# Kernel tuning notes

Hardware: AMD Instinct MI355X
Metric: run time of the kernel (lower is better)

The kernel has to match this reference:

```python
import jax, jax.numpy as jnp
import numpy as np

B, L, R, F, E, H, A, V = 256, 24, 49, 2048, 256, 512, 512, 10000


def setup_inputs() -> dict:
    key = jax.random.key(0)
    ks = jax.random.split(key, 16)
    w = lambda k, shape: jax.random.normal(k, shape, jnp.float32) * 0.02
    feats = jax.random.normal(ks[0], (B, R, F), jnp.float32)
    captions_ids = jax.random.randint(ks[1], (B, L), 0, V).astype(jnp.int32)
    # descending-sorted lengths in [2, L], max forced to L (packed-batch convention)
    lengths = jnp.sort(jax.random.randint(ks[2], (B,), 2, L + 1))[::-1].astype(jnp.int32)
    lengths = lengths.at[0].set(L)
    return {
        "feats": feats,
        "captions_ids": captions_ids,
        "lengths": lengths,
        "embed_W": w(ks[3], (V, E)),
        "Wf": w(ks[4], (A, F)), "bf": jnp.zeros((A,), jnp.float32),
        "Wh": w(ks[5], (A, H)), "bh": jnp.zeros((A,), jnp.float32),
        "Ws": w(ks[6], (1, A)), "bs": jnp.zeros((1,), jnp.float32),
        "W_ih": w(ks[7], (4 * H, E + F)), "b_ih": jnp.zeros((4 * H,), jnp.float32),
        "W_hh": w(ks[8], (4 * H, H)), "b_hh": jnp.zeros((4 * H,), jnp.float32),
        "Wfc": w(ks[9], (V, H)), "bfc": jnp.zeros((V,), jnp.float32),
        "Wi_h": w(ks[10], (H, F)), "bi_h": jnp.zeros((H,), jnp.float32),
        "Wi_c": w(ks[11], (H, F)), "bi_c": jnp.zeros((H,), jnp.float32),
    }


def reference(feats, captions_ids, lengths, embed_W, Wf, bf, Wh, bh, Ws, bs,
              W_ih, b_ih, W_hh, b_hh, Wfc, bfc, Wi_h, bi_h, Wi_c, bi_c):
    # init state from mean-pooled features
    mean = feats.mean(axis=1)                       # (B, F)
    h0 = jnp.tanh(mean @ Wi_h.T + bi_h)             # (B, H)
    c0 = jnp.tanh(mean @ Wi_c.T + bi_c)
    emb = embed_W[captions_ids]                     # (B, L, E)
    f_proj = feats @ Wf.T + bf                      # (B, R, A) hoisted out of loop
    steps = captions_ids.shape[1] - 1

    def step(carry, xs):
        h, c = carry
        emb_t, t = xs                               # (B, E), scalar
        # soft attention
        hp = h @ Wh.T + bh                          # (B, A)
        e = jnp.tanh(f_proj + hp[:, None, :])       # (B, R, A)
        scores = e @ Ws[0] + bs[0]                  # (B, R)
        alpha = jax.nn.softmax(scores, axis=1)
        ctx = jnp.einsum('br,brf->bf', alpha, feats)  # (B, F)
        # LSTMCell (torch gate order i,f,g,o); dropout is identity in eval
        x = jnp.concatenate([emb_t, ctx], axis=1)   # (B, E+F)
        gates = x @ W_ih.T + b_ih + h @ W_hh.T + b_hh
        i, f, g, o = jnp.split(gates, 4, axis=1)
        i, f, o = jax.nn.sigmoid(i), jax.nn.sigmoid(f), jax.nn.sigmoid(o)
        g = jnp.tanh(g)
        c_t = f * c + i * g
        h_t = o * jnp.tanh(c_t)
        # ragged masking: only rows with lengths > t are active this step
        mask = (lengths > t)[:, None]
        h = jnp.where(mask, h_t, h)
        c = jnp.where(mask, c_t, c)
        logit = jnp.where(mask, h_t @ Wfc.T + bfc, 0.0)  # (B, V); zeros for padded rows
        return (h, c), logit

    xs = (jnp.swapaxes(emb[:, :steps], 0, 1), jnp.arange(steps))
    _, logits = jax.lax.scan(step, (h0, c0), xs)    # (steps, B, V)
    return jnp.swapaxes(logits, 0, 1)               # (B, steps, V)
```

## Files before the change

kernel.cpp:

```cpp
#include <hip/hip_runtime.h>

constexpr int Bc = 256, Lc = 24, Rc = 49, Fc = 2048, Ec = 256, Hc = 512, Acn = 512, Vc = 10000;
constexpr int STEPS = Lc - 1;
constexpr int XE = Ec + Fc;
constexpr int NG = 2048 + Acn;
constexpr int VPAD = 10112;

using bf16x8  = __attribute__((ext_vector_type(8))) __bf16;
using floatx4 = __attribute__((ext_vector_type(4))) float;
using ushort8 = __attribute__((ext_vector_type(8))) unsigned short;
using ushort4v = __attribute__((ext_vector_type(4))) unsigned short;

__device__ inline float bf2f(unsigned short u) {
    unsigned int x = ((unsigned int)u) << 16;
    float f; __builtin_memcpy(&f, &x, sizeof(f)); return f;
}
__device__ inline unsigned short f2bf(float f) {
    unsigned int u; __builtin_memcpy(&u, &f, sizeof(u));
    u += 0x7fffu + ((u >> 16) & 1u);
    return (unsigned short)(u >> 16);
}

__device__ inline void gload_lds16(const void* g, void* l) {
    __builtin_amdgcn_global_load_lds(
        (const __attribute__((address_space(1))) unsigned int*)g,
        (__attribute__((address_space(3))) unsigned int*)l, 16, 0, 0);
}

struct CvtArgs {
    const float* src[9];
    unsigned short* dst[9];
};
constexpr int SEG_END[9] = {
    6422528,
    7062528,
    7324672,
    8604672,
    9784320,
    10046464,
    10112000,
    10374144,
    10636288
};
constexpr int CVT_BLOCKS = SEG_END[8] / 256;

__global__ __launch_bounds__(256) void convert_all(CvtArgs a)
{
    int g = blockIdx.x * 256 + threadIdx.x;
    int s = 0, base = 0;
    #pragma unroll
    for (int i = 0; i < 9; i++)
        if (g >= SEG_END[i]) { s = i + 1; }
    if (s >= 9) return;
    base = (s == 0) ? 0 : SEG_END[s - 1];
    const float* sp = a.src[s];
    unsigned short* dp = a.dst[s];
    int off = g - base;
    float4 v = reinterpret_cast<const float4*>(sp)[off];
    ushort4v o;
    o.x = f2bf(v.x); o.y = f2bf(v.y); o.z = f2bf(v.z); o.w = f2bf(v.w);
    reinterpret_cast<ushort4v*>(dp)[off] = o;
}

template <int BM, int BN, int BK, int EPI>
__global__ __launch_bounds__(256) void gemm_tn(
    const unsigned short* __restrict__ A, int lda,
    const unsigned short* __restrict__ Bm, int ldb,
    const unsigned short* __restrict__ Bm2,
    const float* __restrict__ bias,
    const float* __restrict__ bias2,
    float* __restrict__ outF,
    unsigned short* __restrict__ outU,
    float* __restrict__ outF2,
    int N, int K)
{
    static_assert(BK == 64, "row must be 128B for the swizzle");
    __shared__ __align__(16) unsigned short smem[(BM + BN) * BK];
    unsigned short* sA = smem;
    unsigned short* sB = smem + BM * BK;

    const int tid = threadIdx.x;
    const int wid = tid >> 6, lane = tid & 63;
    const int wm = wid >> 1, wn = wid & 1;
    const int m0 = blockIdx.x * BM, n0 = blockIdx.y * BN;
    constexpr int FM = BM / 32, FN = (BN + 31) / 32;
    constexpr int ACH = BM / 32;
    constexpr int BCH = BN / 32;

    floatx4 acc[FM][FN];
    #pragma unroll
    for (int i = 0; i < FM; i++)
        #pragma unroll
        for (int j = 0; j < FN; j++)
            #pragma unroll
            for (int r = 0; r < 4; r++) acc[i][j][r] = 0.f;

    const int lm = lane & 15, half = lane >> 4;
    const int lane16 = lane * 16;

    for (int k0 = 0; k0 < K; k0 += BK) {
        #pragma unroll
        for (int ii = 0; ii < ACH; ii++) {
            int ldso = (wid * ACH + ii) * 1024 + lane16;
            int row = ldso >> 7, colb = ldso & 127;
            int scolb = colb ^ ((row & 7) << 4);
            const char* src = (const char*)(A + (size_t)(m0 + row) * lda + k0) + scolb;
            gload_lds16(src, (char*)sA + ldso);
        }
        #pragma unroll
        for (int ii = 0; ii < BCH; ii++) {
            int ldso = (wid * BCH + ii) * 1024 + lane16;
            int row = ldso >> 7, colb = ldso & 127;
            int scolb = colb ^ ((row & 7) << 4);
            int gn = n0 + row;
            const unsigned short* bp;
            if constexpr (EPI == 2)
                bp = (gn < Hc) ? (Bm + (size_t)gn * ldb) : (Bm2 + (size_t)(gn - Hc) * ldb);
            else
                bp = Bm + (size_t)gn * ldb;
            gload_lds16((const char*)(bp + k0) + scolb, (char*)sB + ldso);
        }
        __syncthreads();

        #pragma unroll
        for (int kk = 0; kk < BK; kk += 32) {
            bf16x8 af[FM], bfb[FN];
            #pragma unroll
            for (int fm = 0; fm < FM; fm++) {
                int ar = wm * (BM / 2) + fm * 16 + lm;
                int ab = ar * 128 + ((kk * 2 + half * 16) ^ ((ar & 7) << 4));
                af[fm] = *reinterpret_cast<const bf16x8*>((const char*)sA + ab);
            }
            #pragma unroll
            for (int fn = 0; fn < FN; fn++) {
                int br = wn * (BN / 2) + fn * 16 + lm;
                int bb = br * 128 + ((kk * 2 + half * 16) ^ ((br & 7) << 4));
                bfb[fn] = *reinterpret_cast<const bf16x8*>((const char*)sB + bb);
            }
            #pragma unroll
            for (int fm = 0; fm < FM; fm++)
                #pragma unroll
                for (int fn = 0; fn < FN; fn++)
                    acc[fm][fn] = __builtin_amdgcn_mfma_f32_16x16x32_bf16(
                        af[fm], bfb[fn], acc[fm][fn], 0, 0, 0);
        }
        __syncthreads();
    }

    const int quad = lane >> 4;
    #pragma unroll
    for (int fm = 0; fm < FM; fm++) {
        #pragma unroll
        for (int fn = 0; fn < FN; fn++) {
            #pragma unroll
            for (int r = 0; r < 4; r++) {
                int rowG = m0 + wm * (BM / 2) + fm * 16 + quad * 4 + r;
                int colG = n0 + wn * (BN / 2) + fn * 16 + lm;
                float v = acc[fm][fn][r];
                if constexpr (EPI == 0) {
                    if (bias) v += bias[colG];
                    outF[(size_t)rowG * N + colG] = v;
                } else if constexpr (EPI == 1) {
                    if (bias) v += bias[colG];
                    outU[(size_t)rowG * N + colG] = f2bf(v);
                } else if constexpr (EPI == 2) {
                    float b = (colG < Hc) ? bias[colG] : bias2[colG - Hc];
                    v = tanhf(v + b);
                    if (colG < Hc) outU[(size_t)rowG * Hc + colG] = f2bf(v);
                    else           outF2[(size_t)rowG * Hc + (colG - Hc)] = v;
                }
            }
        }
    }
}

__global__ __launch_bounds__(256) void logits_gemm(
    const unsigned short* __restrict__ A,
    const unsigned short* __restrict__ Bm,
    const float* __restrict__ bias,
    float* __restrict__ out,
    const int* __restrict__ lengths)
{
    constexpr int BM = 128, BN = 64, BK = 64, K = Hc;
    constexpr int EP = 68;
    __shared__ __align__(16) unsigned char smraw[BM * EP * 4];
    unsigned short* sA = (unsigned short*)smraw;
    unsigned short* sB = sA + BM * BK;
    float* sE = (float*)smraw;

    const int tid = threadIdx.x;
    const int wid = tid >> 6, lane = tid & 63;
    const int wm = wid >> 1, wn = wid & 1;

    constexpr int NWG = 46 * 157, NX = 8;
    constexpr int qq = NWG / NX, rr = NWG % NX;
    int wg = blockIdx.x + blockIdx.y * 46;
    int xcd = wg % NX, i = wg / NX;
    int w = (xcd < rr ? xcd * (qq + 1) : rr * (qq + 1) + (xcd - rr) * qq) + i;
    const int m0 = (w % 46) * BM, n0 = (w / 46) * BN;
    constexpr int FM = 4, FN = 2;

    const int rl = lane >> 4, cl = lane & 15;
    const int colG = n0 + cl * 4;
    const bool colOK = colG < Vc;

    const int tt0 = m0 >> 8;
    if (lengths[m0 & 255] <= tt0) {
        if (colOK) {
            float4 z; z.x = 0.f; z.y = 0.f; z.z = 0.f; z.w = 0.f;
            #pragma unroll
            for (int it = 0; it < 8; it++) {
                int r = wid * 32 + it * 4 + rl;
                int bb = (m0 + r) & 255;
                *reinterpret_cast<float4*>(
                    out + ((size_t)bb * STEPS + tt0) * Vc + colG) = z;
            }
        }
        return;
    }

    floatx4 acc[FM][FN];
    #pragma unroll
    for (int i2 = 0; i2 < FM; i2++)
        #pragma unroll
        for (int j = 0; j < FN; j++)
            #pragma unroll
            for (int r = 0; r < 4; r++) acc[i2][j][r] = 0.f;

    const int lm = lane & 15, half = lane >> 4;
    const int lane16 = lane * 16;

    for (int k0 = 0; k0 < K; k0 += BK) {
        #pragma unroll
        for (int ii = 0; ii < 4; ii++) {
            int ldso = (wid * 4 + ii) * 1024 + lane16;
            int row = ldso >> 7, colb = ldso & 127;
            int scolb = colb ^ ((row & 7) << 4);
            const char* src = (const char*)(A + (size_t)(m0 + row) * K + k0) + scolb;
            gload_lds16(src, (char*)sA + ldso);
        }
        #pragma unroll
        for (int ii = 0; ii < 2; ii++) {
            int ldso = (wid * 2 + ii) * 1024 + lane16;
            int row = ldso >> 7, colb = ldso & 127;
            int scolb = colb ^ ((row & 7) << 4);
            const char* src = (const char*)(Bm + (size_t)(n0 + row) * K + k0) + scolb;
            gload_lds16(src, (char*)sB + ldso);
        }
        __syncthreads();

        #pragma unroll
        for (int kk = 0; kk < BK; kk += 32) {
            bf16x8 af[FM], bfb[FN];
            #pragma unroll
            for (int fm = 0; fm < FM; fm++) {
                int ar = wm * 64 + fm * 16 + lm;
                int ab = ar * 128 + ((kk * 2 + half * 16) ^ ((ar & 7) << 4));
                af[fm] = *reinterpret_cast<const bf16x8*>((const char*)sA + ab);
            }
            #pragma unroll
            for (int fn = 0; fn < FN; fn++) {
                int br = wn * 32 + fn * 16 + lm;
                int bb = br * 128 + ((kk * 2 + half * 16) ^ ((br & 7) << 4));
                bfb[fn] = *reinterpret_cast<const bf16x8*>((const char*)sB + bb);
            }
            #pragma unroll
            for (int fm = 0; fm < FM; fm++)
                #pragma unroll
                for (int fn = 0; fn < FN; fn++)
                    acc[fm][fn] = __builtin_amdgcn_mfma_f32_16x16x32_bf16(
                        af[fm], bfb[fn], acc[fm][fn], 0, 0, 0);
        }
        __syncthreads();
    }

    const int quad = lane >> 4;
    #pragma unroll
    for (int fm = 0; fm < FM; fm++)
        #pragma unroll
        for (int fn = 0; fn < FN; fn++)
            #pragma unroll
            for (int r = 0; r < 4; r++)
                sE[(wm * 64 + fm * 16 + quad * 4 + r) * EP + wn * 32 + fn * 16 + lm]
                    = acc[fm][fn][r];
    __syncthreads();

    if (colOK) {
        float4 bv = *reinterpret_cast<const float4*>(bias + colG);
        #pragma unroll
        for (int it = 0; it < 8; it++) {
            int r = wid * 32 + it * 4 + rl;
            int rowG = m0 + r;
            int tt = rowG >> 8, bb = rowG & 255;
            bool act = lengths[bb] > tt;
            float4 v = *reinterpret_cast<const float4*>(sE + r * EP + cl * 4);
            float4 o;
            o.x = act ? v.x + bv.x : 0.f;
            o.y = act ? v.y + bv.y : 0.f;
            o.z = act ? v.z + bv.z : 0.f;
            o.w = act ? v.w + bv.w : 0.f;
            *reinterpret_cast<float4*>(out + ((size_t)bb * STEPS + tt) * Vc + colG) = o;
        }
    }
}

__global__ __launch_bounds__(256) void attn_lstm_kernel(
    const unsigned short* __restrict__ fproj,
    const unsigned short* __restrict__ fprojG,
    const unsigned short* __restrict__ embProj,
    const float* __restrict__ hg,
    const float* __restrict__ bh,
    const float* __restrict__ Ws,
    const float* __restrict__ bs,
    const float* __restrict__ b_ih,
    const float* __restrict__ b_hh,
    float* __restrict__ c_state,
    unsigned short* __restrict__ h_buf,
    unsigned short* __restrict__ h_all,
    const int* __restrict__ lengths,
    const int* __restrict__ ids,
    int t)
{
    const int b = blockIdx.x, tid = threadIdx.x;
    const int wid = tid >> 6, lane = tid & 63;
    __shared__ float s_hp[Acn];
    __shared__ float s_sc[64];
    __shared__ float s_g[2048];

    #pragma unroll
    for (int i = tid; i < Acn; i += 256)
        s_hp[i] = hg[(size_t)b * NG + 2048 + i] + bh[i];
    __syncthreads();

    float ws8[8], hp8[8];
    {
        const float* wsb = Ws + lane * 8;
        #pragma unroll
        for (int j = 0; j < 8; j++) { ws8[j] = wsb[j]; hp8[j] = s_hp[lane * 8 + j]; }
    }
    for (int r = wid; r < Rc; r += 4) {
        ushort8 e = *reinterpret_cast<const ushort8*>(
            fproj + ((size_t)b * Rc + r) * Acn + lane * 8);
        float sum = 0.f;
        #pragma unroll
        for (int j = 0; j < 8; j++)
            sum += ws8[j] * tanhf(bf2f(e[j]) + hp8[j]);
        #pragma unroll
        for (int off = 32; off > 0; off >>= 1) sum += __shfl_down(sum, off);
        if (lane == 0) s_sc[r] = sum + bs[0];
    }
    __syncthreads();

    if (wid == 0) {
        float v = (lane < Rc) ? s_sc[lane] : -3.0e38f;
        float mx = v;
        #pragma unroll
        for (int off = 32; off > 0; off >>= 1) mx = fmaxf(mx, __shfl_xor(mx, off));
        float e = (lane < Rc) ? __expf(v - mx) : 0.f;
        float sm = e;
        #pragma unroll
        for (int off = 32; off > 0; off >>= 1) sm += __shfl_xor(sm, off);
        if (lane < Rc) s_sc[lane] = e / sm;
    }
    __syncthreads();

    const int g0 = tid * 8;
    const int id = ids[b * Lc + t];
    float g8[8];
    {
        ushort8 ev = *reinterpret_cast<const ushort8*>(embProj + (size_t)id * 2048 + g0);
        const float* hgb = hg + (size_t)b * NG + g0;
        #pragma unroll
        for (int j = 0; j < 8; j++)
            g8[j] = bf2f(ev[j]) + hgb[j] + b_ih[g0 + j] + b_hh[g0 + j];
    }
    #pragma unroll 7
    for (int r = 0; r < Rc; r++) {
        float a = s_sc[r];
        ushort8 v = *reinterpret_cast<const ushort8*>(
            fprojG + ((size_t)b * Rc + r) * 2048 + g0);
        #pragma unroll
        for (int j = 0; j < 8; j++) g8[j] += a * bf2f(v[j]);
    }
    #pragma unroll
    for (int j = 0; j < 8; j++) s_g[g0 + j] = g8[j];
    __syncthreads();

    const bool act = lengths[b] > t;
    #pragma unroll
    for (int jj = 0; jj < 2; jj++) {
        int j = tid * 2 + jj;
        float gi = s_g[j], gf = s_g[Hc + j], gg = s_g[2 * Hc + j], go = s_g[3 * Hc + j];
        float i_ = 1.f / (1.f + __expf(-gi));
        float f_ = 1.f / (1.f + __expf(-gf));
        float gv = tanhf(gg);
        float o_ = 1.f / (1.f + __expf(-go));
        float c_old = c_state[(size_t)b * Hc + j];
        float ct = f_ * c_old + i_ * gv;
        float ht = o_ * tanhf(ct);
        unsigned short hb = f2bf(ht);
        h_all[((size_t)t * Bc + b) * Hc + j] = hb;
        if (act) {
            c_state[(size_t)b * Hc + j] = ct;
            h_buf[(size_t)b * Hc + j] = hb;
        }
    }
}

__global__ __launch_bounds__(256) void mean_kernel(
    const unsigned short* __restrict__ featsB,
    unsigned short* __restrict__ meanB)
{
    const int b = blockIdx.x, tid = threadIdx.x;
    const int f0 = tid * 8;
    float s[8];
    #pragma unroll
    for (int j = 0; j < 8; j++) s[j] = 0.f;
    #pragma unroll 7
    for (int r = 0; r < Rc; r++) {
        ushort8 v = *reinterpret_cast<const ushort8*>(
            featsB + ((size_t)(b * Rc + r)) * Fc + f0);
        #pragma unroll
        for (int j = 0; j < 8; j++) s[j] += bf2f(v[j]);
    }
    ushort8 o;
    #pragma unroll
    for (int j = 0; j < 8; j++) o[j] = f2bf(s[j] * (1.f / (float)Rc));
    *reinterpret_cast<ushort8*>(meanB + (size_t)b * Fc + f0) = o;
}

extern "C" void kernel_launch(void* const* d_in, const int* in_sizes, int n_in,
                              void* d_out, int out_size, void* d_ws, size_t ws_size,
                              hipStream_t stream)
{
    const float* feats = (const float*)d_in[0];
    const int*   ids   = (const int*)d_in[1];
    const int*   lens  = (const int*)d_in[2];
    const float* embW  = (const float*)d_in[3];
    const float* Wf    = (const float*)d_in[4];
    const float* bf_   = (const float*)d_in[5];
    const float* Wh    = (const float*)d_in[6];
    const float* bh    = (const float*)d_in[7];
    const float* Ws_   = (const float*)d_in[8];
    const float* bs_   = (const float*)d_in[9];
    const float* W_ih  = (const float*)d_in[10];
    const float* b_ih  = (const float*)d_in[11];
    const float* W_hh  = (const float*)d_in[12];
    const float* b_hh  = (const float*)d_in[13];
    const float* Wfc   = (const float*)d_in[14];
    const float* bfc   = (const float*)d_in[15];
    const float* Wi_h  = (const float*)d_in[16];
    const float* bi_h  = (const float*)d_in[17];
    const float* Wi_c  = (const float*)d_in[18];
    const float* bi_c  = (const float*)d_in[19];

    char* ws = (char*)d_ws;
    auto alloc_us = [&](size_t n) { unsigned short* p = (unsigned short*)ws; ws += n * 2; return p; };
    auto alloc_f  = [&](size_t n) { float* p = (float*)ws; ws += n * 4; return p; };

    unsigned short* featsB = alloc_us((size_t)Bc * Rc * Fc);
    unsigned short* embB   = alloc_us((size_t)Vc * Ec);
    unsigned short* WfB    = alloc_us((size_t)Acn * Fc);
    unsigned short* WfcB   = alloc_us((size_t)Vc * Hc);
    unsigned short* WihB   = alloc_us((size_t)2048 * XE);
    unsigned short* Whg    = alloc_us((size_t)NG * Hc);
    unsigned short* WihB2  = alloc_us((size_t)Hc * Fc);
    unsigned short* WicB   = alloc_us((size_t)Hc * Fc);
    unsigned short* meanB  = alloc_us((size_t)Bc * Fc);
    unsigned short* fproj  = alloc_us((size_t)Bc * Rc * Acn);
    unsigned short* fprojG = alloc_us((size_t)Bc * Rc * 2048);
    unsigned short* embPrj = alloc_us((size_t)VPAD * 2048);
    unsigned short* h_buf  = alloc_us((size_t)Bc * Hc);
    unsigned short* h_all  = alloc_us((size_t)STEPS * Bc * Hc);
    float*          c_st   = alloc_f((size_t)Bc * Hc);
    float*          hg     = alloc_f((size_t)Bc * NG);
    float*          outF   = (float*)d_out;

    CvtArgs ca;
    ca.src[0] = feats; ca.dst[0] = featsB;
    ca.src[1] = embW;  ca.dst[1] = embB;
    ca.src[2] = Wf;    ca.dst[2] = WfB;
    ca.src[3] = Wfc;   ca.dst[3] = WfcB;
    ca.src[4] = W_ih;  ca.dst[4] = WihB;
    ca.src[5] = W_hh;  ca.dst[5] = Whg;
    ca.src[6] = Wh;    ca.dst[6] = Whg + (size_t)2048 * Hc;
    ca.src[7] = Wi_h;  ca.dst[7] = WihB2;
    ca.src[8] = Wi_c;  ca.dst[8] = WicB;
    convert_all<<<CVT_BLOCKS, 256, 0, stream>>>(ca);

    mean_kernel<<<Bc, 256, 0, stream>>>(featsB, meanB);

    gemm_tn<64, 64, 64, 2><<<dim3(4, 16), 256, 0, stream>>>(
        meanB, Fc, WihB2, Fc, WicB, bi_h, bi_c,
        nullptr, h_buf, c_st, 2 * Hc, Fc);

    gemm_tn<128, 128, 64, 1><<<dim3(98, 4), 256, 0, stream>>>(
        featsB, Fc, WfB, Fc, nullptr, bf_, nullptr,
        nullptr, fproj, nullptr, Acn, Fc);

    gemm_tn<128, 128, 64, 1><<<dim3(98, 16), 256, 0, stream>>>(
        featsB, Fc, WihB + 256, XE, nullptr, nullptr, nullptr,
        nullptr, fprojG, nullptr, 2048, Fc);

    gemm_tn<128, 128, 64, 1><<<dim3(VPAD / 128, 16), 256, 0, stream>>>(
        embB, Ec, WihB, XE, nullptr, nullptr, nullptr,
        nullptr, embPrj, nullptr, 2048, Ec);

    for (int t = 0; t < STEPS; t++) {
        gemm_tn<64, 32, 64, 0><<<dim3(4, 80), 256, 0, stream>>>(
            h_buf, Hc, Whg, Hc, nullptr, nullptr, nullptr,
            hg, nullptr, nullptr, NG, Hc);

        attn_lstm_kernel<<<Bc, 256, 0, stream>>>(
            fproj, fprojG, embPrj, hg, bh, Ws_, bs_, b_ih, b_hh,
            c_st, h_buf, h_all, lens, ids, t);
    }

    logits_gemm<<<dim3(46, 157), 256, 0, stream>>>(
        h_all, WfcB, bfc, outF, lens);
}
```

Measured before the change: 1.493 ms.

## Skip finished sequences in recurrent step kernels and XCD-swizzle precompute GEMMs

Each recurrent step now early-exits any attention/LSTM block whose batch row has already ended. The hidden-projection GEMM also skips any 64-row tile whose first row is inactive, which is valid because lengths are sorted in descending order. This removes recurrent work for padded rows, on the assumption that the logits stage masks those rows on its own, since h_all is no longer written for them. The large precompute GEMMs also get a remap of workgroups to XCDs so neighbouring tiles share each chiplet's L2.

Measured after the change: 1.472 ms. No clear change (-1.4%).

```diff
diff --git a/kernel.cpp b/kernel.cpp
--- a/kernel.cpp
+++ b/kernel.cpp
@@ -62,7 +62,7 @@
     reinterpret_cast<ushort4v*>(dp)[off] = o;
 }
 
-template <int BM, int BN, int BK, int EPI>
+template <int BM, int BN, int BK, int EPI, bool XSWZ = false>
 __global__ __launch_bounds__(256) void gemm_tn(
     const unsigned short* __restrict__ A, int lda,
     const unsigned short* __restrict__ Bm, int ldb,
@@ -72,7 +72,8 @@
     float* __restrict__ outF,
     unsigned short* __restrict__ outU,
     float* __restrict__ outF2,
-    int N, int K)
+    int N, int K,
+    const int* __restrict__ lens, int tcur)
 {
     static_assert(BK == 64, "row must be 128B for the swizzle");
     __shared__ __align__(16) unsigned short smem[(BM + BN) * BK];
@@ -82,7 +83,23 @@
     const int tid = threadIdx.x;
     const int wid = tid >> 6, lane = tid & 63;
     const int wm = wid >> 1, wn = wid & 1;
-    const int m0 = blockIdx.x * BM, n0 = blockIdx.y * BN;
+
+    int bx = blockIdx.x, by = blockIdx.y;
+    if constexpr (XSWZ) {
+        int gx = gridDim.x;
+        int nwg = gx * gridDim.y;
+        int q = nwg >> 3, r = nwg & 7;
+        int wg = bx + by * gx;
+        int xcd = wg & 7, idx = wg >> 3;
+        int w = (xcd < r ? xcd * (q + 1) : r * (q + 1) + (xcd - r) * q) + idx;
+        bx = w % gx; by = w / gx;
+    }
+    const int m0 = bx * BM, n0 = by * BN;
+
+    if constexpr (EPI == 0) {
+        if (lens && lens[m0] <= tcur) return;
+    }
+
     constexpr int FM = BM / 32, FN = (BN + 31) / 32;
     constexpr int ACH = BM / 32;
     constexpr int BCH = BN / 32;
@@ -322,6 +339,8 @@
     int t)
 {
     const int b = blockIdx.x, tid = threadIdx.x;
+    if (lengths[b] <= t) return;
+
     const int wid = tid >> 6, lane = tid & 63;
     __shared__ float s_hp[Acn];
     __shared__ float s_sc[64];
@@ -386,7 +405,6 @@
     for (int j = 0; j < 8; j++) s_g[g0 + j] = g8[j];
     __syncthreads();
 
-    const bool act = lengths[b] > t;
     #pragma unroll
     for (int jj = 0; jj < 2; jj++) {
         int j = tid * 2 + jj;
@@ -400,10 +418,8 @@
         float ht = o_ * tanhf(ct);
         unsigned short hb = f2bf(ht);
         h_all[((size_t)t * Bc + b) * Hc + j] = hb;
-        if (act) {
-            c_state[(size_t)b * Hc + j] = ct;
-            h_buf[(size_t)b * Hc + j] = hb;
-        }
+        c_state[(size_t)b * Hc + j] = ct;
+        h_buf[(size_t)b * Hc + j] = hb;
     }
 }
 
@@ -492,24 +508,24 @@
 
     gemm_tn<64, 64, 64, 2><<<dim3(4, 16), 256, 0, stream>>>(
         meanB, Fc, WihB2, Fc, WicB, bi_h, bi_c,
-        nullptr, h_buf, c_st, 2 * Hc, Fc);
-
-    gemm_tn<128, 128, 64, 1><<<dim3(98, 4), 256, 0, stream>>>(
+        nullptr, h_buf, c_st, 2 * Hc, Fc, nullptr, 0);
+
+    gemm_tn<128, 128, 64, 1, true><<<dim3(98, 4), 256, 0, stream>>>(
         featsB, Fc, WfB, Fc, nullptr, bf_, nullptr,
-        nullptr, fproj, nullptr, Acn, Fc);
-
-    gemm_tn<128, 128, 64, 1><<<dim3(98, 16), 256, 0, stream>>>(
+        nullptr, fproj, nullptr, Acn, Fc, nullptr, 0);
+
+    gemm_tn<128, 128, 64, 1, true><<<dim3(98, 16), 256, 0, stream>>>(
         featsB, Fc, WihB + 256, XE, nullptr, nullptr, nullptr,
-        nullptr, fprojG, nullptr, 2048, Fc);
-
-    gemm_tn<128, 128, 64, 1><<<dim3(VPAD / 128, 16), 256, 0, stream>>>(
+        nullptr, fprojG, nullptr, 2048, Fc, nullptr, 0);
+
+    gemm_tn<128, 128, 64, 1, true><<<dim3(VPAD / 128, 16), 256, 0, stream>>>(
         embB, Ec, WihB, XE, nullptr, nullptr, nullptr,
-        nullptr, embPrj, nullptr, 2048, Ec);
+        nullptr, embPrj, nullptr, 2048, Ec, nullptr, 0);
 
     for (int t = 0; t < STEPS; t++) {
         gemm_tn<64, 32, 64, 0><<<dim3(4, 80), 256, 0, stream>>>(
             h_buf, Hc, Whg, Hc, nullptr, nullptr, nullptr,
-            hg, nullptr, nullptr, NG, Hc);
+            hg, nullptr, nullptr, NG, Hc, lens, t);
 
         attn_lstm_kernel<<<Bc, 256, 0, stream>>>(
             fproj, fprojG, embPrj, hg, bh, Ws_, bs_, b_ih, b_hh,
```

## Skip finished sequences in recurrent GEMM and attention-LSTM, widen LSTM blocks

Applied to the files above, without the earlier changes.

The per-step recurrent GEMM now exits early for row tiles whose first batch row has already finished. Because lengths are sorted in descending order, that means every row in the tile is done. The attention/LSTM kernel also returns immediately for finished batch rows, and now runs 512 threads per block so each thread handles half as many gate elements and region rows. This drops the masked-out recurrent work that was previously computed and then discarded. As a result, h_all rows for finished sequences are left unwritten, and correctness relies on the logits kernel masking those rows and on the sorted-lengths convention.

Measured after the change: 1.292 ms. 13.4% less time.

```diff
diff --git a/kernel.cpp b/kernel.cpp
--- a/kernel.cpp
+++ b/kernel.cpp
@@ -72,7 +72,8 @@
     float* __restrict__ outF,
     unsigned short* __restrict__ outU,
     float* __restrict__ outF2,
-    int N, int K)
+    int N, int K,
+    const int* __restrict__ lens, int tcur)
 {
     static_assert(BK == 64, "row must be 128B for the swizzle");
     __shared__ __align__(16) unsigned short smem[(BM + BN) * BK];
@@ -83,6 +84,11 @@
     const int wid = tid >> 6, lane = tid & 63;
     const int wm = wid >> 1, wn = wid & 1;
     const int m0 = blockIdx.x * BM, n0 = blockIdx.y * BN;
+
+    if constexpr (EPI == 0) {
+        if (lens && lens[m0] <= tcur) return;
+    }
+
     constexpr int FM = BM / 32, FN = (BN + 31) / 32;
     constexpr int ACH = BM / 32;
     constexpr int BCH = BN / 32;
@@ -304,7 +310,7 @@
     }
 }
 
-__global__ __launch_bounds__(256) void attn_lstm_kernel(
+__global__ __launch_bounds__(512) void attn_lstm_kernel(
     const unsigned short* __restrict__ fproj,
     const unsigned short* __restrict__ fprojG,
     const unsigned short* __restrict__ embProj,
@@ -322,14 +328,15 @@
     int t)
 {
     const int b = blockIdx.x, tid = threadIdx.x;
+    if (lengths[b] <= t) return;
+
     const int wid = tid >> 6, lane = tid & 63;
     __shared__ float s_hp[Acn];
     __shared__ float s_sc[64];
     __shared__ float s_g[2048];
 
-    #pragma unroll
-    for (int i = tid; i < Acn; i += 256)
-        s_hp[i] = hg[(size_t)b * NG + 2048 + i] + bh[i];
+    if (tid < Acn)
+        s_hp[tid] = hg[(size_t)b * NG + 2048 + tid] + bh[tid];
     __syncthreads();
 
     float ws8[8], hp8[8];
@@ -338,7 +345,7 @@
         #pragma unroll
         for (int j = 0; j < 8; j++) { ws8[j] = wsb[j]; hp8[j] = s_hp[lane * 8 + j]; }
     }
-    for (int r = wid; r < Rc; r += 4) {
+    for (int r = wid; r < Rc; r += 8) {
         ushort8 e = *reinterpret_cast<const ushort8*>(
             fproj + ((size_t)b * Rc + r) * Acn + lane * 8);
         float sum = 0.f;
@@ -364,32 +371,30 @@
     }
     __syncthreads();
 
-    const int g0 = tid * 8;
+    const int g0 = tid * 4;
     const int id = ids[b * Lc + t];
-    float g8[8];
+    float g4[4];
     {
-        ushort8 ev = *reinterpret_cast<const ushort8*>(embProj + (size_t)id * 2048 + g0);
+        ushort4v ev = *reinterpret_cast<const ushort4v*>(embProj + (size_t)id * 2048 + g0);
         const float* hgb = hg + (size_t)b * NG + g0;
         #pragma unroll
-        for (int j = 0; j < 8; j++)
-            g8[j] = bf2f(ev[j]) + hgb[j] + b_ih[g0 + j] + b_hh[g0 + j];
+        for (int j = 0; j < 4; j++)
+            g4[j] = bf2f(ev[j]) + hgb[j] + b_ih[g0 + j] + b_hh[g0 + j];
     }
     #pragma unroll 7
     for (int r = 0; r < Rc; r++) {
         float a = s_sc[r];
-        ushort8 v = *reinterpret_cast<const ushort8*>(
+        ushort4v v = *reinterpret_cast<const ushort4v*>(
             fprojG + ((size_t)b * Rc + r) * 2048 + g0);
         #pragma unroll
-        for (int j = 0; j < 8; j++) g8[j] += a * bf2f(v[j]);
-    }
-    #pragma unroll
-    for (int j = 0; j < 8; j++) s_g[g0 + j] = g8[j];
+        for (int j = 0; j < 4; j++) g4[j] += a * bf2f(v[j]);
+    }
+    #pragma unroll
+    for (int j = 0; j < 4; j++) s_g[g0 + j] = g4[j];
     __syncthreads();
 
-    const bool act = lengths[b] > t;
-    #pragma unroll
-    for (int jj = 0; jj < 2; jj++) {
-        int j = tid * 2 + jj;
+    if (tid < Hc) {
+        int j = tid;
         float gi = s_g[j], gf = s_g[Hc + j], gg = s_g[2 * Hc + j], go = s_g[3 * Hc + j];
         float i_ = 1.f / (1.f + __expf(-gi));
         float f_ = 1.f / (1.f + __expf(-gf));
@@ -400,10 +405,8 @@
         float ht = o_ * tanhf(ct);
         unsigned short hb = f2bf(ht);
         h_all[((size_t)t * Bc + b) * Hc + j] = hb;
-        if (act) {
-            c_state[(size_t)b * Hc + j] = ct;
-            h_buf[(size_t)b * Hc + j] = hb;
-        }
+        c_state[(size_t)b * Hc + j] = ct;
+        h_buf[(size_t)b * Hc + j] = hb;
     }
 }
 
@@ -492,26 +495,26 @@
 
     gemm_tn<64, 64, 64, 2><<<dim3(4, 16), 256, 0, stream>>>(
         meanB, Fc, WihB2, Fc, WicB, bi_h, bi_c,
-        nullptr, h_buf, c_st, 2 * Hc, Fc);
+        nullptr, h_buf, c_st, 2 * Hc, Fc, nullptr, 0);
 
     gemm_tn<128, 128, 64, 1><<<dim3(98, 4), 256, 0, stream>>>(
         featsB, Fc, WfB, Fc, nullptr, bf_, nullptr,
-        nullptr, fproj, nullptr, Acn, Fc);
+        nullptr, fproj, nullptr, Acn, Fc, nullptr, 0);
 
     gemm_tn<128, 128, 64, 1><<<dim3(98, 16), 256, 0, stream>>>(
         featsB, Fc, WihB + 256, XE, nullptr, nullptr, nullptr,
-        nullptr, fprojG, nullptr, 2048, Fc);
+        nullptr, fprojG, nullptr, 2048, Fc, nullptr, 0);
 
     gemm_tn<128, 128, 64, 1><<<dim3(VPAD / 128, 16), 256, 0, stream>>>(
         embB, Ec, WihB, XE, nullptr, nullptr, nullptr,
-        nullptr, embPrj, nullptr, 2048, Ec);
+        nullptr, embPrj, nullptr, 2048, Ec, nullptr, 0);
 
     for (int t = 0; t < STEPS; t++) {
         gemm_tn<64, 32, 64, 0><<<dim3(4, 80), 256, 0, stream>>>(
             h_buf, Hc, Whg, Hc, nullptr, nullptr, nullptr,
-            hg, nullptr, nullptr, NG, Hc);
-
-        attn_lstm_kernel<<<Bc, 256, 0, stream>>>(
+            hg, nullptr, nullptr, NG, Hc, lens, t);
+
+        attn_lstm_kernel<<<Bc, 512, 0, stream>>>(
             fproj, fprojG, embPrj, hg, bh, Ws_, bs_, b_ih, b_hh,
             c_st, h_buf, h_all, lens, ids, t);
     }
```
